# Optimization experiments

Hardware: AMD Instinct MI355X
Metric: run time of the kernel (lower is better)

Reference implementation:

```python
import jax, jax.numpy as jnp
import numpy as np

K = 24            # neighbors
RBF_KERNELS = 16
RBF_GAMMA = 10.0
CUTOFF = 5.0
BN_EPS = 1e-5


def setup_inputs() -> dict:
    key = jax.random.key(0)
    ks = jax.random.split(key, 6)
    B, C, N = 16, 32, 2048
    x = jax.random.normal(ks[0], (B, C, N), dtype=jnp.float32)
    idx_base = (jnp.arange(B, dtype=jnp.int64) * N).reshape(B, 1, 1)
    att_w1 = jax.random.normal(ks[1], (64, 2 * C + RBF_KERNELS), dtype=jnp.float32) * 0.1
    att_w2 = jax.random.normal(ks[2], (1, 64), dtype=jnp.float32) * 0.1
    upd_w = jax.random.normal(ks[3], (64, C), dtype=jnp.float32) * 0.1
    bn_gamma = jnp.ones((64,), dtype=jnp.float32)
    bn_beta = jnp.zeros((64,), dtype=jnp.float32)
    res_w = jax.random.normal(ks[4], (64, C), dtype=jnp.float32) * 0.1
    return {"x": x, "idx_base": idx_base, "att_w1": att_w1, "att_w2": att_w2,
            "upd_w": upd_w, "bn_gamma": bn_gamma, "bn_beta": bn_beta, "res_w": res_w}


def _forward(x, att_w1, att_w2, upd_w, bn_gamma, bn_beta, res_w):
    B, C, N = x.shape
    centers = jnp.linspace(0.0, CUTOFF, RBF_KERNELS).astype(x.dtype)
    # pair[b,i,j] = -||x_i - x_j||^2  (negative squared distance)
    xx = jnp.sum(x * x, axis=1)                          # [B,N]
    dots = jnp.einsum('bcn,bcm->bnm', x, x)              # [B,N,N]
    pair = 2.0 * dots - xx[:, :, None] - xx[:, None, :]
    neg_d2, idx = jax.lax.top_k(pair, K)                 # [B,N,K] nearest neighbors
    dist = jnp.sqrt(jnp.maximum(-neg_d2, 1e-12))         # [B,N,K]
    xt = jnp.transpose(x, (0, 2, 1))                     # [B,N,C]
    neigh = xt[jnp.arange(B)[:, None, None], idx]        # [B,N,K,C] gather
    cent = jnp.broadcast_to(xt[:, :, None, :], (B, N, K, C))
    # RBF expansion of neighbor distances
    diff = dist[..., None] - centers                     # [B,N,K,RBF]
    rbf = jnp.clip(jnp.exp(-RBF_GAMMA * diff * diff), 1e-10, 1.0)
    # attention MLP (1x1 convs == per-edge dense layers)
    att_in = jnp.concatenate([cent, neigh, rbf], axis=-1)          # [B,N,K,2C+RBF]
    h = jax.nn.leaky_relu(jnp.einsum('bnkf,of->bnko', att_in, att_w1), 0.2)
    logits = jnp.einsum('bnko,o->bnk', h, att_w2[0])               # [B,N,K]
    att = jax.nn.softmax(logits, axis=-1)                          # softmax over K neighbors
    weighted = att[..., None] * neigh                              # [B,N,K,C]
    # update_ff: conv1x1 -> BatchNorm2d (batch stats over B,N,K) -> LeakyReLU(0.02)
    upd = jnp.einsum('bnkc,oc->bnko', weighted, upd_w)             # [B,N,K,64]
    mean = jnp.mean(upd, axis=(0, 1, 2))
    var = jnp.mean((upd - mean) ** 2, axis=(0, 1, 2))
    upd = (upd - mean) * jax.lax.rsqrt(var + BN_EPS) * bn_gamma + bn_beta
    upd = jax.nn.leaky_relu(upd, 0.02)
    res = jnp.einsum('bnkc,oc->bnko', neigh, res_w)                # residual projection
    feat = jnp.mean(upd + 0.1 * res, axis=2)                       # mean over K -> [B,N,64]
    return jnp.transpose(feat, (0, 2, 1))                          # [B,64,N]


def reference(x, idx_base, att_w1, att_w2, upd_w, bn_gamma, bn_beta, res_w):
    # idx_base is only needed for torch's flattened-gather trick; the per-batch
    # advanced-index gather above computes identical math.
    return _forward(x, att_w1, att_w2, upd_w, bn_gamma, bn_beta, res_w)
```

## Files before the change

kernel.cpp:

```cpp
#include <hip/hip_runtime.h>
#include <math.h>

#define B_   16
#define C_   32
#define N_   2048
#define K_   24
#define BNK_ (B_*N_*K_)

typedef float vf2 __attribute__((ext_vector_type(2)));
typedef __attribute__((ext_vector_type(8))) short bf16x8;
typedef __attribute__((ext_vector_type(4))) float f32x4;

#define WS_XT   0u
#define WS_XXD  1048576u
#define WS_XXF  1114112u
#define WS_IDX  1146880u
#define WS_D2   1933312u
#define WS_ATT  2719744u
#define WS_LOG  3506176u
#define WS_ST   4292608u
#define WS_AB   4292736u
#define WS_W    4292864u
#define WS_W2   4325632u
#define WS_Y    4358400u
#define WS_L    4358400u
#define WS_HL   10649856u

__device__ __forceinline__ unsigned short bf16rne(float f) {
  unsigned int u = __float_as_uint(f);
  return (unsigned short)((u + 0x7FFFu + ((u >> 16) & 1u)) >> 16);
}

#define DPP_ADD(p, ctrl, rm)                                                  \
  (p) += __int_as_float(__builtin_amdgcn_update_dpp(                          \
      0, __float_as_int(p), (ctrl), (rm), 0xf, true))

__global__ __launch_bounds__(256) void k0_prep(const float* __restrict__ x,
                                               float* __restrict__ ws) {
  const int i = blockIdx.x;
  const int xcd = i & 7, j = i >> 3;
  const int b = 2 * xcd + (j & 1);
  const int half = j >> 1;
  const int t = (b << 11) + (half << 8) + threadIdx.x;
  const int n = t & 2047;
  const float* xp = x + ((size_t)b * C_ * N_) + n;
  float4* xt4 = (float4*)(ws + WS_XT + (size_t)t * C_);
  uint4*  hl  = (uint4*)(ws + WS_HL) + (size_t)t * 8;
  unsigned int hu[16], lu[16];
  double s = 0.0;
#pragma unroll
  for (int cg = 0; cg < 8; ++cg) {
    float4 v;
    v.x = xp[(size_t)(4*cg  ) * N_];
    v.y = xp[(size_t)(4*cg+1) * N_];
    v.z = xp[(size_t)(4*cg+2) * N_];
    v.w = xp[(size_t)(4*cg+3) * N_];
    xt4[cg] = v;
    s = fma((double)v.x, (double)v.x, s);
    s = fma((double)v.y, (double)v.y, s);
    s = fma((double)v.z, (double)v.z, s);
    s = fma((double)v.w, (double)v.w, s);
    unsigned short h0 = bf16rne(v.x), h1 = bf16rne(v.y);
    unsigned short h2 = bf16rne(v.z), h3 = bf16rne(v.w);
    float l0 = v.x - __uint_as_float((unsigned int)h0 << 16);
    float l1 = v.y - __uint_as_float((unsigned int)h1 << 16);
    float l2 = v.z - __uint_as_float((unsigned int)h2 << 16);
    float l3 = v.w - __uint_as_float((unsigned int)h3 << 16);
    hu[2*cg]   = (unsigned int)h0 | ((unsigned int)h1 << 16);
    hu[2*cg+1] = (unsigned int)h2 | ((unsigned int)h3 << 16);
    lu[2*cg]   = (unsigned int)bf16rne(l0) | ((unsigned int)bf16rne(l1) << 16);
    lu[2*cg+1] = (unsigned int)bf16rne(l2) | ((unsigned int)bf16rne(l3) << 16);
  }
#pragma unroll
  for (int q = 0; q < 4; ++q) {
    uint4 hv; hv.x = hu[4*q]; hv.y = hu[4*q+1]; hv.z = hu[4*q+2]; hv.w = hu[4*q+3];
    hl[q] = hv;
    uint4 lv; lv.x = lu[4*q]; lv.y = lu[4*q+1]; lv.z = lu[4*q+2]; lv.w = lu[4*q+3];
    hl[4+q] = lv;
  }
  ((double*)(ws + WS_XXD))[t] = s;
  ws[WS_XXF + t] = -0.5f * (float)s;
  ws[WS_W + t] = 0.f;
  ws[WS_W2 + t] = 0.f;
  if (t < 128) ws[WS_ST + t] = 0.f;
}

__global__ __launch_bounds__(256, 8) void k1a_mfma(float* __restrict__ ws) {
  __shared__ unsigned short tl[2][1024];
  const int lane = threadIdx.x & 63;
  const int wv   = __builtin_amdgcn_readfirstlane(threadIdx.x >> 6);
  const int i = blockIdx.x;
  const int xcd = i & 7, j = i >> 3;
  const int b = 2 * xcd + (j & 1);
  const int j2 = j >> 1;
  const int nblk = j2 >> 2;
  const int mq   = j2 & 3;
  const int l16 = lane & 15, lg = lane >> 4;

  const unsigned short* HL = (const unsigned short*)(ws + WS_HL) + ((size_t)b << 17);
  const int nrow = (nblk << 6) + (wv << 4) + l16;
  const bf16x8 bh = *(const bf16x8*)(HL + ((size_t)nrow << 6) + (lg << 3));
  const bf16x8 bl = *(const bf16x8*)(HL + ((size_t)nrow << 6) + 32 + (lg << 3));

  const int mbase = mq << 9;
  const float4* nxx = (const float4*)(ws + WS_XXF + (b << 11) + mbase);

  const int srow = lane >> 3;
  const int sslot = (lane & 7) ^ srow;
  const unsigned short* Sp = HL + ((size_t)(mbase + srow) << 6) + (sslot << 3);

  const int ah_off = (l16 << 6) + (((lg    ) ^ (l16 & 7)) << 3);
  const int al_off = (l16 << 6) + (((4 | lg) ^ (l16 & 7)) << 3);

  if (wv == 0) {
    __builtin_amdgcn_global_load_lds(
        (const __attribute__((address_space(1))) unsigned int*)(const void*)Sp,
        (__attribute__((address_space(3))) unsigned int*)(void*)&tl[0][0], 16, 0, 0);
    __builtin_amdgcn_global_load_lds(
        (const __attribute__((address_space(1))) unsigned int*)(const void*)(Sp + 512),
        (__attribute__((address_space(3))) unsigned int*)(void*)&tl[0][512], 16, 0, 0);
  }
  __syncthreads();

  float val[12];
#pragma unroll
  for (int j0 = 0; j0 < 12; ++j0) val[j0] = -3.4e38f;
  int id = mbase + (lg << 2);

#pragma unroll 2
  for (int t = 0; t < 32; ++t) {
    const int cur = t & 1;
    if (t < 31 && wv == (t & 3)) {
      const unsigned short* sp = Sp + ((size_t)(t + 1) << 10);
      __builtin_amdgcn_global_load_lds(
          (const __attribute__((address_space(1))) unsigned int*)(const void*)sp,
          (__attribute__((address_space(3))) unsigned int*)(void*)&tl[cur ^ 1][0], 16, 0, 0);
      __builtin_amdgcn_global_load_lds(
          (const __attribute__((address_space(1))) unsigned int*)(const void*)(sp + 512),
          (__attribute__((address_space(3))) unsigned int*)(void*)&tl[cur ^ 1][512], 16, 0, 0);
    }
    bf16x8 ah = *(const bf16x8*)(&tl[cur][ah_off]);
    bf16x8 al = *(const bf16x8*)(&tl[cur][al_off]);
    float4 xq = nxx[(t << 2) + lg];
    f32x4 acc;
    acc[0] = xq.x; acc[1] = xq.y; acc[2] = xq.z; acc[3] = xq.w;
    acc = __builtin_amdgcn_mfma_f32_16x16x32_bf16(ah, bh, acc, 0, 0, 0);
    acc = __builtin_amdgcn_mfma_f32_16x16x32_bf16(al, bh, acc, 0, 0, 0);
    acc = __builtin_amdgcn_mfma_f32_16x16x32_bf16(ah, bl, acc, 0, 0, 0);
#pragma unroll
    for (int r = 0; r < 4; ++r) {
      int sb = (__float_as_int(acc[r]) & ~2047) | (id + r);
      float sp2 = __int_as_float(sb);
#pragma unroll
      for (int j0 = 11; j0 >= 1; --j0)
        val[j0] = __builtin_amdgcn_fmed3f(val[j0 - 1], val[j0], sp2);
      val[0] = fmaxf(val[0], sp2);
    }
    id += 16;
    __syncthreads();
  }
  const int pg = (b << 5) + nblk;
  float* Lp = ws + WS_L +
      (((size_t)pg * 16 + (mq << 2) + lg) * 12) * 64 + (wv << 4) + l16;
#pragma unroll
  for (int j0 = 0; j0 < 12; ++j0) Lp[(size_t)j0 * 64] = val[j0];
}

__global__ __launch_bounds__(64) void k1b_sel(float* __restrict__ ws) {
  const float* xt = ws + WS_XT;
  const double* xxd = (const double*)(ws + WS_XXD);
  const int lane = threadIdx.x & 63;
  const int i = blockIdx.x;
  const int xcd = i & 7, j = i >> 3;
  const int b = 2 * xcd + (j & 1);
  const int sub = j >> 1;
  const int pg = (b << 5) + sub;
  const int bn = (b << 11) + (sub << 6) + lane;

  float val[28];
#pragma unroll
  for (int j0 = 0; j0 < 28; ++j0) val[j0] = -3.4e38f;
  const float* Lp = ws + WS_L + ((size_t)pg * 16 * 12) * 64 + lane;
#pragma unroll 4
  for (int t = 0; t < 192; ++t) {
    float sp = Lp[(size_t)t * 64];
#pragma unroll
    for (int j0 = 27; j0 >= 1; --j0)
      val[j0] = __builtin_amdgcn_fmed3f(val[j0 - 1], val[j0], sp);
    val[0] = fmaxf(val[0], sp);
  }

  double xnd[C_];
  {
    const float* p = xt + (size_t)bn * C_;
#pragma unroll
    for (int c = 0; c < C_; ++c) xnd[c] = (double)p[c];
  }
  double dl[K_];
#pragma unroll
  for (int j0 = 0; j0 < K_; ++j0) dl[j0] = -1.7e308;

#pragma unroll 1
  for (int j0 = 0; j0 < 28; ++j0) {
    const int m = __float_as_int(val[j0]) & 2047;
    const float* r = xt + ((size_t)((b << 11) + m)) * C_;
    double a0 = 0.0, a1 = 0.0;
#pragma unroll
    for (int c = 0; c < 16; ++c) {
      a0 = fma((double)r[c],      xnd[c],      a0);
      a1 = fma((double)r[c + 16], xnd[c + 16], a1);
    }
    double s = 2.0 * (a0 + a1) - xxd[(b << 11) + m];
    long long bits = (__double_as_longlong(s) & 0xFFFFFFFFFFFFF800ll) | (long long)m;
    double sp = __longlong_as_double(bits);
    if (sp > dl[K_ - 1]) {
      bool c2 = true;
#pragma unroll
      for (int jj = K_ - 1; jj >= 1; --jj) {
        bool c1 = sp > dl[jj - 1];
        dl[jj] = c1 ? dl[jj - 1] : (c2 ? sp : dl[jj]);
        c2 = c1;
      }
      if (c2) dl[0] = sp;
    }
  }

  int*   op = (int*)ws + WS_IDX + (size_t)bn * K_;
  float* dp = ws + WS_D2 + (size_t)bn * K_;
  const double xxn = xxd[bn];
#pragma unroll
  for (int rr = 0; rr < K_; ++rr) {
    long long bl = __double_as_longlong(dl[rr]);
    op[rr] = (int)(bl & 0x7FFll);
    dp[rr] = (float)(xxn - __longlong_as_double(bl & 0xFFFFFFFFFFFFF800ll));
  }
}

__global__ __launch_bounds__(256) void kY(const float* __restrict__ w1,
                                          const float* __restrict__ updw,
                                          const float* __restrict__ resw,
                                          float* __restrict__ ws) {
  const int lane = threadIdx.x & 63;
  const int wv   = __builtin_amdgcn_readfirstlane(threadIdx.x >> 6);
  const int i = blockIdx.x;
  const int xcd = i & 7, j = i >> 3;
  const int b = 2 * xcd + (j & 1);
  const int j2 = j >> 1;
  const int slot = (j2 << 2) | wv;
  const int s  = slot & 7;
  const int pg = slot >> 3;
  const int p = (b << 11) + (pg << 6) + lane;
  const float* xt = ws + WS_XT;

  float row[C_];
  {
    const float4* rp = (const float4*)(xt + (size_t)p * C_);
#pragma unroll
    for (int q = 0; q < 8; ++q) {
      float4 v = rp[q];
      row[4*q] = v.x; row[4*q+1] = v.y; row[4*q+2] = v.z; row[4*q+3] = v.w;
    }
  }
  const int part = s >> 1;
  const int hch  = (s & 1) * 32;
  const float* W   = (part == 0) ? w1 : (part == 1) ? (w1 + 32)
                   : (part == 2) ? updw : resw;
  const int stride = (part < 2) ? 80 : 32;
  float* yp = ws + WS_Y + (size_t)p * 256 + s * 32;
#pragma unroll 2
  for (int og = 0; og < 8; ++og) {
    float a[4] = {0.f, 0.f, 0.f, 0.f};
#pragma unroll
    for (int u = 0; u < 4; ++u) {
      const float* wr = W + (hch + 4 * og + u) * stride;
#pragma unroll
      for (int c = 0; c < C_; ++c) a[u] = fmaf(row[c], wr[c], a[u]);
    }
    float4 st; st.x = a[0]; st.y = a[1]; st.z = a[2]; st.w = a[3];
    ((float4*)yp)[og] = st;
  }
}

__global__ __launch_bounds__(256, 8) void k2_logits(const float* __restrict__ w1,
                                                    const float* __restrict__ w2,
                                                    float* __restrict__ ws) {
  __shared__ float dist_s[4][24];
  __shared__ float rbf_s[4][384];
  const int lane = threadIdx.x & 63;
  const int wv   = __builtin_amdgcn_readfirstlane(threadIdx.x >> 6);
  const int i = blockIdx.x;
  const int xcd = i & 7, j = i >> 3;
  const int b = 2 * xcd + (j & 1);
  const int grp = j >> 1;
  const float* Y = ws + WS_Y;

  float w1r[16], w2r;
  {
    const float4* wp = (const float4*)(w1 + lane * 80 + 64);
#pragma unroll
    for (int q = 0; q < 4; ++q) {
      float4 v = wp[q];
      w1r[4*q] = v.x; w1r[4*q+1] = v.y; w1r[4*q+2] = v.z; w1r[4*q+3] = v.w;
    }
    w2r = w2[lane];
  }

#pragma unroll 1
  for (int q = 0; q < 4; ++q) {
    const int bn = (b << 11) + (grp << 4) + (wv << 2) + q;
    const int*   ip  = (const int*)ws + WS_IDX + (size_t)bn * K_;
    const float* dpp = ws + WS_D2 + (size_t)bn * K_;
    if (lane < K_) dist_s[wv][lane] = sqrtf(fmaxf(dpp[lane], 1e-12f));
#pragma unroll
    for (int t = 0; t < 6; ++t) {
      const int f = lane + (t << 6);
      const int k = f >> 4, r = f & 15;
      float d = dist_s[wv][k];
      float tt = d - (float)r * (5.0f / 15.0f);
      float e = __expf(-10.f * tt * tt);
      rbf_s[wv][f] = fminf(fmaxf(e, 1e-10f), 1.0f);
    }
    const float ba = Y[(size_t)bn * 256 + lane];
#pragma unroll 2
    for (int k = 0; k < K_; ++k) {
      const int mk = ip[k];
      float rv = Y[(size_t)((b << 11) + mk) * 256 + 64 + lane];
      const float4* rp = (const float4*)&rbf_s[wv][k << 4];
      float4 r0 = rp[0], r1 = rp[1], r2 = rp[2], r3 = rp[3];
      float acc = ba + rv;
      acc = fmaf(r0.x, w1r[0],  acc); acc = fmaf(r0.y, w1r[1],  acc);
      acc = fmaf(r0.z, w1r[2],  acc); acc = fmaf(r0.w, w1r[3],  acc);
      acc = fmaf(r1.x, w1r[4],  acc); acc = fmaf(r1.y, w1r[5],  acc);
      acc = fmaf(r1.z, w1r[6],  acc); acc = fmaf(r1.w, w1r[7],  acc);
      acc = fmaf(r2.x, w1r[8],  acc); acc = fmaf(r2.y, w1r[9],  acc);
      acc = fmaf(r2.z, w1r[10], acc); acc = fmaf(r2.w, w1r[11], acc);
      acc = fmaf(r3.x, w1r[12], acc); acc = fmaf(r3.y, w1r[13], acc);
      acc = fmaf(r3.z, w1r[14], acc); acc = fmaf(r3.w, w1r[15], acc);
      acc = fmaxf(acc, 0.2f * acc);
      float p = acc * w2r;
      DPP_ADD(p, 0xB1,  0xf);
      DPP_ADD(p, 0x4E,  0xf);
      DPP_ADD(p, 0x141, 0xf);
      DPP_ADD(p, 0x140, 0xf);
      DPP_ADD(p, 0x142, 0xa);
      DPP_ADD(p, 0x143, 0xc);
      if (lane == 63) ws[WS_LOG + (size_t)k * 32768 + bn] = p;
    }
  }
}

__global__ __launch_bounds__(256) void k2_softmax(float* __restrict__ ws) {
  __shared__ float h[4096];
  const int i = blockIdx.x;
  const int xcd = i & 7, j = i >> 3;
  const int b = 2 * xcd + (j & 1);
  const int half = j >> 1;
  const int bn = (b << 11) + (half << 8) + threadIdx.x;

#pragma unroll
  for (int q = 0; q < 16; ++q) h[threadIdx.x + (q << 8)] = 0.f;
  __syncthreads();

  float l[K_];
#pragma unroll
  for (int k = 0; k < K_; ++k) l[k] = ws[WS_LOG + (size_t)k * 32768 + bn];
  float mx = l[0];
#pragma unroll
  for (int k = 1; k < K_; ++k) mx = fmaxf(mx, l[k]);
  float den = 0.f;
#pragma unroll
  for (int k = 0; k < K_; ++k) { l[k] = __expf(l[k] - mx); den += l[k]; }
  const float inv = 1.f / den;
#pragma unroll
  for (int k = 0; k < K_; ++k) l[k] *= inv;

  float4* ap = (float4*)(ws + WS_ATT + (size_t)bn * K_);
#pragma unroll
  for (int q = 0; q < 6; ++q) {
    float4 v; v.x = l[4*q]; v.y = l[4*q+1]; v.z = l[4*q+2]; v.w = l[4*q+3];
    ap[q] = v;
  }
  const int* ip = (const int*)ws + WS_IDX + (size_t)bn * K_;
#pragma unroll
  for (int k = 0; k < K_; ++k) {
    const int mk = ip[k];
    atomicAdd(&h[mk], l[k]);
    atomicAdd(&h[2048 + mk], l[k] * l[k]);
  }
  __syncthreads();
#pragma unroll
  for (int q = 0; q < 8; ++q) {
    const int m = threadIdx.x + (q << 8);
    atomicAdd(ws + WS_W  + (b << 11) + m, h[m]);
    atomicAdd(ws + WS_W2 + (b << 11) + m, h[2048 + m]);
  }
}

__global__ __launch_bounds__(256) void k2b_stats(float* __restrict__ ws) {
  __shared__ float ls[128];
  const int lane = threadIdx.x & 63;
  const int wv   = __builtin_amdgcn_readfirstlane(threadIdx.x >> 6);
  if (threadIdx.x < 128) ls[threadIdx.x] = 0.f;
  __syncthreads();
  const int i = blockIdx.x;
  const int xcd = i & 7, j = i >> 3;
  const int b = 2 * xcd + (j & 1);
  const int half = j >> 1;
  const float* Y = ws + WS_Y;
  float s1 = 0.f, s2 = 0.f;
#pragma unroll 1
  for (int it = 0; it < 64; ++it) {
    const int m = (b << 11) + (half << 8) + (wv << 6) + it;
    const float w  = ws[WS_W + m];
    const float w2 = ws[WS_W2 + m];
    const float yv = Y[(size_t)m * 256 + 128 + lane];
    s1 = fmaf(w, yv, s1);
    s2 = fmaf(w2, yv * yv, s2);
  }
  atomicAdd(&ls[lane], s1);
  atomicAdd(&ls[64 + lane], s2);
  __syncthreads();
  if (threadIdx.x < 128) atomicAdd(ws + WS_ST + threadIdx.x, ls[threadIdx.x]);
}

__global__ __launch_bounds__(256) void k4_out(float* __restrict__ out,
                                              const float* __restrict__ gam,
                                              const float* __restrict__ bet,
                                              const float* __restrict__ ws) {
  __shared__ float tile[32][65];
  const int lane = threadIdx.x & 63;
  const int wv   = __builtin_amdgcn_readfirstlane(threadIdx.x >> 6);
  const int i = blockIdx.x;
  const int xcd = i & 7, j = i >> 3;
  const int b = 2 * xcd + (j & 1);
  const int j2 = j >> 1;
  const int n0 = j2 << 5;
  const float* Y = ws + WS_Y;

  float A, Bb;
  {
    const float s1 = ws[WS_ST + lane], s2 = ws[WS_ST + 64 + lane];
    const float cnt = (float)BNK_;
    const float mean = s1 / cnt;
    const float var = fmaxf(s2 / cnt - mean * mean, 0.f);
    A = gam[lane] / sqrtf(var + 1e-5f);
    Bb = bet[lane] - mean * A;
  }

#pragma unroll 1
  for (int pt = 0; pt < 8; ++pt) {
    const int bn = (b << 11) + n0 + (wv << 3) + pt;
    const int*   ip = (const int*)ws + WS_IDX + (size_t)bn * K_;
    const float* ap = ws + WS_ATT + (size_t)bn * K_;
    float facc = 0.f, racc = 0.f;
#pragma unroll
    for (int k = 0; k < K_; ++k) {
      const int mk = ip[k];
      const float* row = Y + (size_t)((b << 11) + mk) * 256;
      float yv = row[128 + lane];
      float rv = row[192 + lane];
      float u = ap[k] * yv;
      float v = fmaf(u, A, Bb);
      v = v > 0.f ? v : 0.02f * v;
      facc += v;
      racc += rv;
    }
    tile[(wv << 3) + pt][lane] = (facc + 0.1f * racc) * (1.f / 24.f);
  }
  __syncthreads();
  const int o = threadIdx.x >> 2, q = threadIdx.x & 3;
  float* op = out + ((size_t)(b * 64 + o)) * 2048 + n0 + q * 8;
  float4 v0, v1;
  v0.x = tile[q*8+0][o]; v0.y = tile[q*8+1][o]; v0.z = tile[q*8+2][o]; v0.w = tile[q*8+3][o];
  v1.x = tile[q*8+4][o]; v1.y = tile[q*8+5][o]; v1.z = tile[q*8+6][o]; v1.w = tile[q*8+7][o];
  ((float4*)op)[0] = v0;
  ((float4*)op)[1] = v1;
}

extern "C" void kernel_launch(void* const* d_in, const int* in_sizes, int n_in,
                              void* d_out, int out_size, void* d_ws, size_t ws_size,
                              hipStream_t stream) {
  (void)in_sizes; (void)n_in; (void)out_size; (void)ws_size;
  const float* x    = (const float*)d_in[0];
  const float* w1   = (const float*)d_in[2];
  const float* w2   = (const float*)d_in[3];
  const float* updw = (const float*)d_in[4];
  const float* bng  = (const float*)d_in[5];
  const float* bnb  = (const float*)d_in[6];
  const float* resw = (const float*)d_in[7];
  float* out = (float*)d_out;
  float* ws  = (float*)d_ws;

  k0_prep  <<<dim3(128),  dim3(256), 0, stream>>>(x, ws);
  k1a_mfma <<<dim3(2048), dim3(256), 0, stream>>>(ws);
  k1b_sel  <<<dim3(512),  dim3(64),  0, stream>>>(ws);
  kY       <<<dim3(1024), dim3(256), 0, stream>>>(w1, updw, resw, ws);
  k2_logits<<<dim3(2048), dim3(256), 0, stream>>>(w1, w2, ws);
  k2_softmax<<<dim3(128), dim3(256), 0, stream>>>(ws);
  k2b_stats<<<dim3(128),  dim3(256), 0, stream>>>(ws);
  k4_out   <<<dim3(1024), dim3(256), 0, stream>>>(out, bng, bnb, ws);
}
```

Baseline: 313.2 us.

## Compute RBF attention-logit projection with split-bf16 MFMA instead of scalar FMAs

Rewrites the k2_logits per-edge RBF projection (16 RBF features times 64 hidden units) to use 16x16x32 bf16 MFMA instructions, with a hi/lo bf16 split of both operands (three MFMAs) to keep close to fp32 accuracy. RBF values are packed into a swizzled LDS tile per wave, and neighbor rows are processed in tiles of 16 edges. It then reduces across the 16 lanes within each group with DPP adds. It aims to cut the VALU FMA work and the scalar LDS rbf reads. In exchange it lowers occupancy (launch bound 8 to 6), uses more LDS, pads K=24 up to 32, and brings small precision differences.

```diff
diff --git a/kernel.cpp b/kernel.cpp
--- a/kernel.cpp
+++ b/kernel.cpp
@@ -281,70 +281,116 @@
   }
 }
 
-__global__ __launch_bounds__(256, 8) void k2_logits(const float* __restrict__ w1,
+__global__ __launch_bounds__(256, 6) void k2_logits(const float* __restrict__ w1,
                                                     const float* __restrict__ w2,
                                                     float* __restrict__ ws) {
+  __shared__ unsigned short A_s[4][2048];
   __shared__ float dist_s[4][24];
-  __shared__ float rbf_s[4][384];
   const int lane = threadIdx.x & 63;
   const int wv   = __builtin_amdgcn_readfirstlane(threadIdx.x >> 6);
+  const int l16 = lane & 15, lg = lane >> 4;
   const int i = blockIdx.x;
   const int xcd = i & 7, j = i >> 3;
   const int b = 2 * xcd + (j & 1);
   const int grp = j >> 1;
   const float* Y = ws + WS_Y;
 
-  float w1r[16], w2r;
   {
-    const float4* wp = (const float4*)(w1 + lane * 80 + 64);
-#pragma unroll
-    for (int q = 0; q < 4; ++q) {
-      float4 v = wp[q];
-      w1r[4*q] = v.x; w1r[4*q+1] = v.y; w1r[4*q+2] = v.z; w1r[4*q+3] = v.w;
-    }
-    w2r = w2[lane];
+    uint4 z; z.x = 0; z.y = 0; z.z = 0; z.w = 0;
+    uint4* az = (uint4*)&A_s[wv][0];
+    az[lane] = z; az[lane + 64] = z; az[lane + 128] = z; az[lane + 192] = z;
+  }
+
+  bf16x8 w1h[4], w1l[4];
+  float w2r[4];
+#pragma unroll
+  for (int t = 0; t < 4; ++t) {
+    const int o = t * 16 + l16;
+    w2r[t] = w2[o];
+    bf16x8 vh, vl;
+#pragma unroll
+    for (int jj = 0; jj < 8; ++jj) {
+      const int r = lg * 8 + jj;
+      float v = (r < 16) ? w1[o * 80 + 64 + r] : 0.f;
+      unsigned short h = bf16rne(v);
+      float lo = v - __uint_as_float((unsigned int)h << 16);
+      vh[jj] = (short)h;
+      vl[jj] = (short)bf16rne(lo);
+    }
+    w1h[t] = vh; w1l[t] = vl;
   }
 
 #pragma unroll 1
   for (int q = 0; q < 4; ++q) {
     const int bn = (b << 11) + (grp << 4) + (wv << 2) + q;
-    const int*   ip  = (const int*)ws + WS_IDX + (size_t)bn * K_;
     const float* dpp = ws + WS_D2 + (size_t)bn * K_;
     if (lane < K_) dist_s[wv][lane] = sqrtf(fmaxf(dpp[lane], 1e-12f));
 #pragma unroll
-    for (int t = 0; t < 6; ++t) {
-      const int f = lane + (t << 6);
-      const int k = f >> 4, r = f & 15;
-      float d = dist_s[wv][k];
-      float tt = d - (float)r * (5.0f / 15.0f);
-      float e = __expf(-10.f * tt * tt);
-      rbf_s[wv][f] = fminf(fmaxf(e, 1e-10f), 1.0f);
-    }
-    const float ba = Y[(size_t)bn * 256 + lane];
-#pragma unroll 2
-    for (int k = 0; k < K_; ++k) {
-      const int mk = ip[k];
-      float rv = Y[(size_t)((b << 11) + mk) * 256 + 64 + lane];
-      const float4* rp = (const float4*)&rbf_s[wv][k << 4];
-      float4 r0 = rp[0], r1 = rp[1], r2 = rp[2], r3 = rp[3];
-      float acc = ba + rv;
-      acc = fmaf(r0.x, w1r[0],  acc); acc = fmaf(r0.y, w1r[1],  acc);
-      acc = fmaf(r0.z, w1r[2],  acc); acc = fmaf(r0.w, w1r[3],  acc);
-      acc = fmaf(r1.x, w1r[4],  acc); acc = fmaf(r1.y, w1r[5],  acc);
-      acc = fmaf(r1.z, w1r[6],  acc); acc = fmaf(r1.w, w1r[7],  acc);
-      acc = fmaf(r2.x, w1r[8],  acc); acc = fmaf(r2.y, w1r[9],  acc);
-      acc = fmaf(r2.z, w1r[10], acc); acc = fmaf(r2.w, w1r[11], acc);
-      acc = fmaf(r3.x, w1r[12], acc); acc = fmaf(r3.y, w1r[13], acc);
-      acc = fmaf(r3.z, w1r[14], acc); acc = fmaf(r3.w, w1r[15], acc);
-      acc = fmaxf(acc, 0.2f * acc);
-      float p = acc * w2r;
-      DPP_ADD(p, 0xB1,  0xf);
-      DPP_ADD(p, 0x4E,  0xf);
-      DPP_ADD(p, 0x141, 0xf);
-      DPP_ADD(p, 0x140, 0xf);
-      DPP_ADD(p, 0x142, 0xa);
-      DPP_ADD(p, 0x143, 0xc);
-      if (lane == 63) ws[WS_LOG + (size_t)k * 32768 + bn] = p;
+    for (int t = 0; t < 3; ++t) {
+      const int f2 = lane + (t << 6);
+      const int k = f2 >> 3, r2 = f2 & 7;
+      const float d = dist_s[wv][k];
+      float d0 = d - (float)(2 * r2    ) * (5.0f / 15.0f);
+      float d1 = d - (float)(2 * r2 + 1) * (5.0f / 15.0f);
+      float e0 = fminf(fmaxf(__expf(-10.f * d0 * d0), 1e-10f), 1.0f);
+      float e1 = fminf(fmaxf(__expf(-10.f * d1 * d1), 1e-10f), 1.0f);
+      unsigned short h0 = bf16rne(e0), h1 = bf16rne(e1);
+      float lo0 = e0 - __uint_as_float((unsigned int)h0 << 16);
+      float lo1 = e1 - __uint_as_float((unsigned int)h1 << 16);
+      unsigned short g0 = bf16rne(lo0), g1 = bf16rne(lo1);
+      const int slot = r2 >> 2;
+      const int us = (2 * r2) & 7;
+      const int ph = (slot     ^ (k & 7));
+      const int pl = ((4|slot) ^ (k & 7));
+      *(unsigned int*)&A_s[wv][(k << 6) + (ph << 3) + us] =
+          (unsigned int)h0 | ((unsigned int)h1 << 16);
+      *(unsigned int*)&A_s[wv][(k << 6) + (pl << 3) + us] =
+          (unsigned int)g0 | ((unsigned int)g1 << 16);
+    }
+    float ba[4];
+#pragma unroll
+    for (int t = 0; t < 4; ++t) ba[t] = Y[(size_t)bn * 256 + t * 16 + l16];
+
+#pragma unroll
+    for (int kt = 0; kt < 2; ++kt) {
+      const int row = kt * 16 + l16;
+      bf16x8 ah = *(const bf16x8*)&A_s[wv][(row << 6) + (((lg    ) ^ (row & 7)) << 3)];
+      bf16x8 al = *(const bf16x8*)&A_s[wv][(row << 6) + (((4 | lg) ^ (row & 7)) << 3)];
+      int mk[4];
+#pragma unroll
+      for (int reg = 0; reg < 4; ++reg) {
+        const int k = kt * 16 + (lg << 2) + reg;
+        mk[reg] = ((const int*)ws)[WS_IDX + (size_t)bn * K_ + (k < K_ ? k : 0)] & 2047;
+      }
+      float sum[4] = {0.f, 0.f, 0.f, 0.f};
+#pragma unroll
+      for (int t = 0; t < 4; ++t) {
+        f32x4 acc;
+#pragma unroll
+        for (int reg = 0; reg < 4; ++reg) {
+          float rv = Y[(size_t)((b << 11) + mk[reg]) * 256 + 64 + t * 16 + l16];
+          acc[reg] = ba[t] + rv;
+        }
+        acc = __builtin_amdgcn_mfma_f32_16x16x32_bf16(ah, w1h[t], acc, 0, 0, 0);
+        acc = __builtin_amdgcn_mfma_f32_16x16x32_bf16(al, w1h[t], acc, 0, 0, 0);
+        acc = __builtin_amdgcn_mfma_f32_16x16x32_bf16(ah, w1l[t], acc, 0, 0, 0);
+#pragma unroll
+        for (int reg = 0; reg < 4; ++reg) {
+          float a = acc[reg];
+          a = fmaxf(a, 0.2f * a);
+          sum[reg] = fmaf(a, w2r[t], sum[reg]);
+        }
+      }
+#pragma unroll
+      for (int reg = 0; reg < 4; ++reg) {
+        float p = sum[reg];
+        DPP_ADD(p, 0xB1,  0xf);
+        DPP_ADD(p, 0x4E,  0xf);
+        DPP_ADD(p, 0x141, 0xf);
+        DPP_ADD(p, 0x140, 0xf);
+        const int k = kt * 16 + (lg << 2) + reg;
+        if (l16 == 0 && k < K_) ws[WS_LOG + (size_t)k * 32768 + bn] = p;
+      }
     }
   }
 }
```

Result: slower. 376.4 us (+20.1%).
